# Optimization experiments

Measured on AMD Instinct MI355X. Metric: run time of the kernel, lower is better.

Reference implementation:

```python
import jax, jax.numpy as jnp
import numpy as np

PAA_SIZE = 64  # init_kwargs paa_size
GAF_TYPE = 'GADF'  # init_kwargs GAF_type


def setup_inputs() -> dict:
    key = jax.random.key(0)
    x = jax.random.uniform(key, (256, 4096, 32), dtype=jnp.float32)
    return {"x": x}


def reference(x):
    # x: [B, T, C]
    B, T, C = x.shape
    # --- rescale: per-sample, per-channel min-max over time axis -> [0, 1]
    x_min = jnp.min(x, axis=1, keepdims=True)
    x_max = jnp.max(x, axis=1, keepdims=True)
    r = (x - x_min) / (x_max - x_min)            # [B, T, C]
    # --- PAA: strided mean over bins of length size = T // paa_size
    size = T // PAA_SIZE
    p = r[:, : PAA_SIZE * size].reshape(B, PAA_SIZE, size, C).sum(axis=2) / size  # [B, P, C]
    # --- GAF construction
    y = jnp.sqrt(1.0 - p * p)                    # [B, P, C]
    if GAF_TYPE == 'GASF':
        # out[b,i,j,c] = x_i x_j - y_i y_j (symmetric)
        out = jnp.einsum('bic,bjc->bijc', p, p) - jnp.einsum('bic,bjc->bijc', y, y)
    else:  # 'GADF'
        # original: -transpose(y x^T - x y^T) => out[b,i,j,c] = y_i x_j - x_i y_j
        out = jnp.einsum('bic,bjc->bijc', y, p) - jnp.einsum('bic,bjc->bijc', p, y)
    return out  # [B, paa_size, paa_size, C]
```

## Files before the change

### kernel.cpp

```cpp
#include <hip/hip_runtime.h>
#include <math.h>


#define BB   256
#define TT   4096
#define CC   32
#define PP   64
#define PSTR 33

typedef float f32x4 __attribute__((ext_vector_type(4)));

#define SUM_OFF    0
#define SUM_FLOATS (BB * PP * CC)
#define MN_OFF     SUM_FLOATS
#define MM_FLOATS  (BB * 16 * CC)
#define MX_OFF     (MN_OFF + MM_FLOATS)
#define WS_FLOATS  (MX_OFF + MM_FLOATS)
#define WS_BYTES   (WS_FLOATS * 4)

__device__ __forceinline__ float4 f4min(float4 a, float4 b) {
    return make_float4(fminf(a.x,b.x), fminf(a.y,b.y), fminf(a.z,b.z), fminf(a.w,b.w));
}
__device__ __forceinline__ float4 f4max(float4 a, float4 b) {
    return make_float4(fmaxf(a.x,b.x), fmaxf(a.y,b.y), fmaxf(a.z,b.z), fmaxf(a.w,b.w));
}
__device__ __forceinline__ void f4add(float4& a, float4 v) {
    a.x += v.x; a.y += v.y; a.z += v.z; a.w += v.w;
}
__device__ __forceinline__ float4 shflxor4(float4 v, int m) {
    return make_float4(__shfl_xor(v.x, m), __shfl_xor(v.y, m),
                       __shfl_xor(v.z, m), __shfl_xor(v.w, m));
}
__device__ __forceinline__ float4 ntload4(const float4* src) {
    f32x4 t = __builtin_nontemporal_load((const f32x4*)src);
    return make_float4(t.x, t.y, t.z, t.w);
}

__global__ __launch_bounds__(256, 4) void gaf_stats(const float* __restrict__ x,
                                                    float* __restrict__ ws) {
    __shared__ float4 cmn[4][4][8];
    __shared__ float4 cmx[4][4][8];

    const int tid  = threadIdx.x;
    const int lane = tid & 63;
    const int wave = tid >> 6;
    const int cg   = lane & 7;
    const int blk  = blockIdx.x;
    const int W    = blk * 4 + wave;
    const int s    = W & 63;
    const int bofs = W >> 6;

    const float4* xb = (const float4*)x + (size_t)W * 512 + lane;

    float4 mnS[4], mxS[4];

    #pragma unroll
    for (int u = 0; u < 4; ++u) {
        const float4* g = xb + (size_t)u * 2097152;
        float4 buf[8];
        #pragma unroll
        for (int v = 0; v < 8; ++v) buf[v] = ntload4(&g[v * 64]);

        float4 mn = buf[0], mx = buf[0], acc = buf[0];
        #pragma unroll
        for (int v = 1; v < 8; ++v) {
            mn = f4min(mn, buf[v]); mx = f4max(mx, buf[v]); f4add(acc, buf[v]);
        }
        #pragma unroll
        for (int m = 8; m <= 32; m <<= 1) {
            mn = f4min(mn, shflxor4(mn, m));
            mx = f4max(mx, shflxor4(mx, m));
            f4add(acc, shflxor4(acc, m));
        }
        mnS[u] = mn; mxS[u] = mx;

        if (lane < 8) {
            const int b = u * 64 + bofs;
            *(float4*)&ws[SUM_OFF + b * (PP * CC) + s * CC + cg * 4] = acc;
        }
    }

    if (lane < 8) {
        #pragma unroll
        for (int u = 0; u < 4; ++u) { cmn[wave][u][cg] = mnS[u]; cmx[wave][u][cg] = mxS[u]; }
    }
    __syncthreads();

    if (wave < 2 && lane < 32) {
        const int u = lane >> 3, c = lane & 7;
        const int b = u * 64 + bofs;
        if (wave == 0) {
            float4 m = f4min(f4min(cmn[0][u][c], cmn[1][u][c]),
                             f4min(cmn[2][u][c], cmn[3][u][c]));
            *(float4*)&ws[MN_OFF + b * (16 * CC) + (blk & 15) * CC + c * 4] = m;
        } else {
            float4 m = f4max(f4max(cmx[0][u][c], cmx[1][u][c]),
                             f4max(cmx[2][u][c], cmx[3][u][c]));
            *(float4*)&ws[MX_OFF + b * (16 * CC) + (blk & 15) * CC + c * 4] = m;
        }
    }
}

__global__ __launch_bounds__(256, 4) void gaf_outer(const float* __restrict__ ws,
                                                    float* __restrict__ out) {
    __shared__ float sp[PP * PSTR];
    __shared__ float sy[PP * PSTR];
    __shared__ float4 lmn[32];
    __shared__ float4 lmx[32];

    const int tid  = threadIdx.x;
    const int lane = tid & 63;
    const int wave = tid >> 6;
    const int cg   = lane & 7;
    const int blk  = blockIdx.x;
    const int b    = blk >> 2;
    const int i0   = (blk & 3) * 16;

    {
        const int r = (wave & 1) * 8 + (lane >> 3);
        float4 mnk = *(const float4*)&ws[MN_OFF + b * (16 * CC) + r * CC + cg * 4];
        float4 mxk = *(const float4*)&ws[MX_OFF + b * (16 * CC) + r * CC + cg * 4];
        #pragma unroll
        for (int m = 8; m <= 32; m <<= 1) {
            mnk = f4min(mnk, shflxor4(mnk, m));
            mxk = f4max(mxk, shflxor4(mxk, m));
        }
        if (lane < 8) { lmn[wave * 8 + cg] = mnk; lmx[wave * 8 + cg] = mxk; }
    }
    __syncthreads();

    {
        const int cq = tid & 7;
        float4 mnf = f4min(f4min(lmn[cq], lmn[8 + cq]), f4min(lmn[16 + cq], lmn[24 + cq]));
        float4 mxf = f4max(f4max(lmx[cq], lmx[8 + cq]), f4max(lmx[16 + cq], lmx[24 + cq]));
        float4 inv;
        inv.x = 1.0f / (mxf.x - mnf.x);  inv.y = 1.0f / (mxf.y - mnf.y);
        inv.z = 1.0f / (mxf.z - mnf.z);  inv.w = 1.0f / (mxf.w - mnf.w);
        const float s64 = 1.0f / 64.0f;
        #pragma unroll
        for (int h = 0; h < 2; ++h) {
            const int s = (tid >> 3) + h * 32;
            float4 sum = *(const float4*)&ws[SUM_OFF + b * (PP * CC) + s * CC + cq * 4];
            float4 p, y;
            p.x = (sum.x * s64 - mnf.x) * inv.x;  p.y = (sum.y * s64 - mnf.y) * inv.y;
            p.z = (sum.z * s64 - mnf.z) * inv.z;  p.w = (sum.w * s64 - mnf.w) * inv.w;
            y.x = sqrtf(fmaxf(1.f - p.x * p.x, 0.f));  y.y = sqrtf(fmaxf(1.f - p.y * p.y, 0.f));
            y.z = sqrtf(fmaxf(1.f - p.z * p.z, 0.f));  y.w = sqrtf(fmaxf(1.f - p.w * p.w, 0.f));
            *(float4*)&sp[s * PSTR + cq * 4] = p;
            *(float4*)&sy[s * PSTR + cq * 4] = y;
        }
    }
    __syncthreads();

    const int jrow = lane >> 3;
    float4 pj[8], yj[8];
    #pragma unroll
    for (int jc = 0; jc < 8; ++jc) {
        const int j = jc * 8 + jrow;
        pj[jc] = *(const float4*)&sp[j * PSTR + cg * 4];
        yj[jc] = *(const float4*)&sy[j * PSTR + cg * 4];
    }

    float4* ob = (float4*)out + (size_t)b * (PP * PP * CC / 4) + lane;

    #pragma unroll
    for (int ii = 0; ii < 4; ++ii) {
        const int i = i0 + wave * 4 + ii;
        const float4 pi = *(const float4*)&sp[i * PSTR + cg * 4];
        const float4 yi = *(const float4*)&sy[i * PSTR + cg * 4];
        #pragma unroll
        for (int jc = 0; jc < 8; ++jc) {
            float4 r;
            r.x = yi.x * pj[jc].x - pi.x * yj[jc].x;
            r.y = yi.y * pj[jc].y - pi.y * yj[jc].y;
            r.z = yi.z * pj[jc].z - pi.z * yj[jc].z;
            r.w = yi.w * pj[jc].w - pi.w * yj[jc].w;
            ob[i * 512 + jc * 64] = r;
        }
    }
}

__global__ __launch_bounds__(1024, 4) void gaf_fused(const float* __restrict__ x,
                                                     float* __restrict__ out) {
    __shared__ float sp[PP * PSTR];
    __shared__ float sy[PP * PSTR];
    __shared__ float redmin[16 * CC];
    __shared__ float redmax[16 * CC];

    const int tid  = threadIdx.x;
    const int lane = tid & 63;
    const int wave = tid >> 6;
    const int cg   = lane & 7;
    const int b    = blockIdx.x;

    const float4* xw = (const float4*)x + (size_t)b * (TT * CC / 4) + wave * 2048 + lane;

    const float FBIG = 3.402823466e+38f;
    float4 mn = make_float4(FBIG, FBIG, FBIG, FBIG);
    float4 mx = make_float4(-FBIG, -FBIG, -FBIG, -FBIG);
    float4 acc[4];
    #pragma unroll
    for (int g = 0; g < 4; ++g) acc[g] = make_float4(0.f, 0.f, 0.f, 0.f);

    #pragma unroll
    for (int g = 0; g < 4; ++g) {
        float4 buf[8];
        #pragma unroll
        for (int u = 0; u < 8; ++u) buf[u] = xw[(g * 8 + u) * 64];
        #pragma unroll
        for (int u = 0; u < 8; ++u) {
            mn = f4min(mn, buf[u]); mx = f4max(mx, buf[u]); f4add(acc[g], buf[u]);
        }
    }

    #pragma unroll
    for (int m = 8; m <= 32; m <<= 1) {
        mn = f4min(mn, shflxor4(mn, m));
        mx = f4max(mx, shflxor4(mx, m));
        #pragma unroll
        for (int g = 0; g < 4; ++g) f4add(acc[g], shflxor4(acc[g], m));
    }

    if (lane < 8) {
        *(float4*)&redmin[wave * CC + cg * 4] = mn;
        *(float4*)&redmax[wave * CC + cg * 4] = mx;
    }
    __syncthreads();

    float4 gmn = *(const float4*)&redmin[0 * CC + cg * 4];
    float4 gmx = *(const float4*)&redmax[0 * CC + cg * 4];
    #pragma unroll
    for (int w = 1; w < 16; ++w) {
        gmn = f4min(gmn, *(const float4*)&redmin[w * CC + cg * 4]);
        gmx = f4max(gmx, *(const float4*)&redmax[w * CC + cg * 4]);
    }

    float4 inv;
    inv.x = 1.0f / (gmx.x - gmn.x);  inv.y = 1.0f / (gmx.y - gmn.y);
    inv.z = 1.0f / (gmx.z - gmn.z);  inv.w = 1.0f / (gmx.w - gmn.w);
    const float s64 = 1.0f / 64.0f;

    if (lane < 8) {
        #pragma unroll
        for (int g = 0; g < 4; ++g) {
            float4 p, y;
            p.x = (acc[g].x * s64 - gmn.x) * inv.x;  p.y = (acc[g].y * s64 - gmn.y) * inv.y;
            p.z = (acc[g].z * s64 - gmn.z) * inv.z;  p.w = (acc[g].w * s64 - gmn.w) * inv.w;
            y.x = sqrtf(fmaxf(1.f - p.x * p.x, 0.f));  y.y = sqrtf(fmaxf(1.f - p.y * p.y, 0.f));
            y.z = sqrtf(fmaxf(1.f - p.z * p.z, 0.f));  y.w = sqrtf(fmaxf(1.f - p.w * p.w, 0.f));
            const int s = wave * 4 + g;
            *(float4*)&sp[s * PSTR + cg * 4] = p;
            *(float4*)&sy[s * PSTR + cg * 4] = y;
        }
    }
    __syncthreads();

    const int jrow = lane >> 3;
    float4 pj[8], yj[8];
    #pragma unroll
    for (int jc = 0; jc < 8; ++jc) {
        const int j = jc * 8 + jrow;
        pj[jc] = *(const float4*)&sp[j * PSTR + cg * 4];
        yj[jc] = *(const float4*)&sy[j * PSTR + cg * 4];
    }

    float4* ob = (float4*)out + (size_t)b * (PP * PP * CC / 4) + wave * 2048 + lane;

    #pragma unroll
    for (int ii = 0; ii < 4; ++ii) {
        const float4 pi = *(const float4*)&sp[(wave * 4 + ii) * PSTR + cg * 4];
        const float4 yi = *(const float4*)&sy[(wave * 4 + ii) * PSTR + cg * 4];
        #pragma unroll
        for (int jc = 0; jc < 8; ++jc) {
            float4 r;
            r.x = yi.x * pj[jc].x - pi.x * yj[jc].x;
            r.y = yi.y * pj[jc].y - pi.y * yj[jc].y;
            r.z = yi.z * pj[jc].z - pi.z * yj[jc].z;
            r.w = yi.w * pj[jc].w - pi.w * yj[jc].w;
            ob[ii * 512 + jc * 64] = r;
        }
    }
}

extern "C" void kernel_launch(void* const* d_in, const int* in_sizes, int n_in,
                              void* d_out, int out_size, void* d_ws, size_t ws_size,
                              hipStream_t stream) {
    const float* x = (const float*)d_in[0];
    float* out = (float*)d_out;
    if (d_ws != nullptr && ws_size >= (size_t)WS_BYTES) {
        float* ws = (float*)d_ws;
        gaf_stats<<<1024, 256, 0, stream>>>(x, ws);
        gaf_outer<<<BB * 4, 256, 0, stream>>>(ws, out);
    } else {
        gaf_fused<<<BB, 1024, 0, stream>>>(x, out);
    }
}
```

Baseline: 221.5 us.

## Split outer-product stage into finalize and nontemporal-store write kernels

Replaces the combined outer kernel with two kernels. A per-batch finalize kernel converts the PAA sums into normalized p values in place in the workspace. A separate write kernel reads p straight from global memory, recomputes y on the fly, and streams the output with nontemporal stores, using a larger grid and higher occupancy. The aim is to cut the LDS staging and redundant min/max reduction done per output block and to speed up the output-bound write phase, at the cost of an extra kernel launch and repeated p loads and sqrt computations.

```diff
diff --git a/kernel.cpp b/kernel.cpp
--- a/kernel.cpp
+++ b/kernel.cpp
@@ -34,6 +34,16 @@
 __device__ __forceinline__ float4 ntload4(const float4* src) {
     f32x4 t = __builtin_nontemporal_load((const f32x4*)src);
     return make_float4(t.x, t.y, t.z, t.w);
+}
+__device__ __forceinline__ void ntstore4(float4* dst, float4 v) {
+    f32x4 t; t.x = v.x; t.y = v.y; t.z = v.z; t.w = v.w;
+    __builtin_nontemporal_store(t, (f32x4*)dst);
+}
+__device__ __forceinline__ float4 f4y(float4 p) {
+    return make_float4(sqrtf(fmaxf(1.f - p.x*p.x, 0.f)),
+                       sqrtf(fmaxf(1.f - p.y*p.y, 0.f)),
+                       sqrtf(fmaxf(1.f - p.z*p.z, 0.f)),
+                       sqrtf(fmaxf(1.f - p.w*p.w, 0.f)));
 }
 
 __global__ __launch_bounds__(256, 4) void gaf_stats(const float* __restrict__ x,
@@ -101,10 +111,7 @@
     }
 }
 
-__global__ __launch_bounds__(256, 4) void gaf_outer(const float* __restrict__ ws,
-                                                    float* __restrict__ out) {
-    __shared__ float sp[PP * PSTR];
-    __shared__ float sy[PP * PSTR];
+__global__ __launch_bounds__(256, 4) void gaf_finalize(float* __restrict__ ws) {
     __shared__ float4 lmn[32];
     __shared__ float4 lmx[32];
 
@@ -112,9 +119,7 @@
     const int lane = tid & 63;
     const int wave = tid >> 6;
     const int cg   = lane & 7;
-    const int blk  = blockIdx.x;
-    const int b    = blk >> 2;
-    const int i0   = (blk & 3) * 16;
+    const int b    = blockIdx.x;
 
     {
         const int r = (wave & 1) * 8 + (lane >> 3);
@@ -140,42 +145,55 @@
         #pragma unroll
         for (int h = 0; h < 2; ++h) {
             const int s = (tid >> 3) + h * 32;
-            float4 sum = *(const float4*)&ws[SUM_OFF + b * (PP * CC) + s * CC + cq * 4];
-            float4 p, y;
+            float* addr = &ws[SUM_OFF + b * (PP * CC) + s * CC + cq * 4];
+            float4 sum = *(const float4*)addr;
+            float4 p;
             p.x = (sum.x * s64 - mnf.x) * inv.x;  p.y = (sum.y * s64 - mnf.y) * inv.y;
             p.z = (sum.z * s64 - mnf.z) * inv.z;  p.w = (sum.w * s64 - mnf.w) * inv.w;
-            y.x = sqrtf(fmaxf(1.f - p.x * p.x, 0.f));  y.y = sqrtf(fmaxf(1.f - p.y * p.y, 0.f));
-            y.z = sqrtf(fmaxf(1.f - p.z * p.z, 0.f));  y.w = sqrtf(fmaxf(1.f - p.w * p.w, 0.f));
-            *(float4*)&sp[s * PSTR + cq * 4] = p;
-            *(float4*)&sy[s * PSTR + cq * 4] = y;
-        }
-    }
-    __syncthreads();
-
-    const int jrow = lane >> 3;
-    float4 pj[8], yj[8];
-    #pragma unroll
-    for (int jc = 0; jc < 8; ++jc) {
-        const int j = jc * 8 + jrow;
-        pj[jc] = *(const float4*)&sp[j * PSTR + cg * 4];
-        yj[jc] = *(const float4*)&sy[j * PSTR + cg * 4];
-    }
-
-    float4* ob = (float4*)out + (size_t)b * (PP * PP * CC / 4) + lane;
-
-    #pragma unroll
-    for (int ii = 0; ii < 4; ++ii) {
-        const int i = i0 + wave * 4 + ii;
-        const float4 pi = *(const float4*)&sp[i * PSTR + cg * 4];
-        const float4 yi = *(const float4*)&sy[i * PSTR + cg * 4];
-        #pragma unroll
-        for (int jc = 0; jc < 8; ++jc) {
-            float4 r;
-            r.x = yi.x * pj[jc].x - pi.x * yj[jc].x;
-            r.y = yi.y * pj[jc].y - pi.y * yj[jc].y;
-            r.z = yi.z * pj[jc].z - pi.z * yj[jc].z;
-            r.w = yi.w * pj[jc].w - pi.w * yj[jc].w;
-            ob[i * 512 + jc * 64] = r;
+            *(float4*)addr = p;
+        }
+    }
+}
+
+__global__ __launch_bounds__(256, 8) void gaf_write(const float* __restrict__ ws,
+                                                    float* __restrict__ out) {
+    const int tid  = threadIdx.x;
+    const int lane = tid & 63;
+    const int wave = tid >> 6;
+    const int cg   = lane & 7;
+    const int lr   = lane >> 3;
+    const int blk  = blockIdx.x;
+
+    #pragma unroll
+    for (int iter = 0; iter < 2; ++iter) {
+        const int g = iter * 8192 + blk * 4 + wave;
+        const int b = g >> 6;
+        const int i = g & 63;
+        const float* Pb = ws + SUM_OFF + b * (PP * CC);
+
+        const float4 pi = *(const float4*)&Pb[i * CC + cg * 4];
+        const float4 yi = f4y(pi);
+
+        float4* ob = (float4*)out + (size_t)b * (PP * PP * CC / 4) + i * 512 + lane;
+
+        #pragma unroll
+        for (int gq = 0; gq < 2; ++gq) {
+            float4 pj[4];
+            #pragma unroll
+            for (int q = 0; q < 4; ++q) {
+                const int j = (gq * 4 + q) * 8 + lr;
+                pj[q] = *(const float4*)&Pb[j * CC + cg * 4];
+            }
+            #pragma unroll
+            for (int q = 0; q < 4; ++q) {
+                const float4 yj = f4y(pj[q]);
+                float4 r;
+                r.x = yi.x * pj[q].x - pi.x * yj.x;
+                r.y = yi.y * pj[q].y - pi.y * yj.y;
+                r.z = yi.z * pj[q].z - pi.z * yj.z;
+                r.w = yi.w * pj[q].w - pi.w * yj.w;
+                ntstore4(&ob[(gq * 4 + q) * 64], r);
+            }
         }
     }
 }
@@ -290,7 +308,8 @@
     if (d_ws != nullptr && ws_size >= (size_t)WS_BYTES) {
         float* ws = (float*)d_ws;
         gaf_stats<<<1024, 256, 0, stream>>>(x, ws);
-        gaf_outer<<<BB * 4, 256, 0, stream>>>(ws, out);
+        gaf_finalize<<<BB, 256, 0, stream>>>(ws);
+        gaf_write<<<2048, 256, 0, stream>>>(ws, out);
     } else {
         gaf_fused<<<BB, 1024, 0, stream>>>(x, out);
     }
```

Result: no change. 224.8 us (+1.5%).
